# Performance work log

Hardware: AMD Instinct MI355X
Metric: run time of the kernel (lower is better)

The kernel has to match this reference:

```python
import jax, jax.numpy as jnp
import numpy as np

N, E, F, S, R, H = 10000, 160000, 128, 10, 8, 64
SH_OFF = [0, 1, 4, 9]
SH_DIM = [1, 3, 5, 7]
AVG_NUM_NEIGHBORS = 16.0


def setup_inputs() -> dict:
    key = jax.random.key(0)
    ks = jax.random.split(key, 16)
    species = jax.random.randint(ks[0], (N,), 0, S)
    node_attrs = jax.nn.one_hot(species, S, dtype=jnp.float32)
    node_feats = jax.random.normal(ks[1], (N, F), dtype=jnp.float32)
    edge_attrs = jax.random.normal(ks[2], (E, 16), dtype=jnp.float32)
    edge_feats = jax.random.normal(ks[3], (E, R), dtype=jnp.float32)
    edge_index = jax.random.randint(ks[4], (2, E), 0, N)
    # learned parameters
    W_skip_node = jax.random.normal(ks[5], (F, S, F), dtype=jnp.float32)
    W_up = jax.random.normal(ks[6], (F, F), dtype=jnp.float32)
    mlp_w1 = jax.random.normal(ks[7], (R, H), dtype=jnp.float32)
    mlp_w2 = jax.random.normal(ks[8], (H, H), dtype=jnp.float32)
    mlp_w3 = jax.random.normal(ks[9], (H, H), dtype=jnp.float32)
    mlp_w4 = jax.random.normal(ks[10], (H, 4 * F), dtype=jnp.float32)  # conv_tp.weight_numel = 512
    W_lin = jax.random.normal(ks[11], (4, F, F), dtype=jnp.float32)
    W_skip_msg = jax.random.normal(ks[12], (4, F, S, F), dtype=jnp.float32)
    W_out = jax.random.normal(ks[13], (F, F), dtype=jnp.float32)
    return dict(node_attrs=node_attrs, node_feats=node_feats, edge_attrs=edge_attrs,
                edge_feats=edge_feats, edge_index=edge_index, species=species,
                W_skip_node=W_skip_node, W_up=W_up, mlp_w1=mlp_w1, mlp_w2=mlp_w2,
                mlp_w3=mlp_w3, mlp_w4=mlp_w4, W_lin=W_lin, W_skip_msg=W_skip_msg,
                W_out=W_out)


def reference(node_attrs, node_feats, edge_attrs, edge_feats, edge_index, species,
              W_skip_node, W_up, mlp_w1, mlp_w2, mlp_w3, mlp_w4,
              W_lin, W_skip_msg, W_out):
    sender, receiver = edge_index[0], edge_index[1]
    num_nodes = node_feats.shape[0]
    num_edges = edge_attrs.shape[0]

    # skip_tp_node: FullyConnectedTensorProduct(128x0e, 10x0e -> 128x0e), fan_in = 128*10
    skip = jnp.einsum('nu,nv,uvw->nw', node_feats, node_attrs, W_skip_node) * (1.0 / np.sqrt(F * S))

    # linear_up: 128x0e -> 128x0e
    h = (node_feats @ W_up) * (1.0 / np.sqrt(F))

    # radial MLP (e3nn FullyConnectedNet: no bias, w/sqrt(fan_in), silu on hidden layers)
    t = edge_feats
    for W in (mlp_w1, mlp_w2, mlp_w3):
        t = jax.nn.silu((t @ W) * (1.0 / np.sqrt(W.shape[0])))
    tp_w = (t @ mlp_w4) * (1.0 / np.sqrt(H))  # [E, 512]

    # conv_tp (gather -> 0e x l -> l 'uvu' TP) fused with scatter_sum per l-block
    hs = h[sender]  # [E, 128]
    msgs = []
    for l in range(4):
        d = SH_DIM[l]
        w_l = tp_w[:, l * F:(l + 1) * F]                       # [E, 128]
        sh_l = edge_attrs[:, SH_OFF[l]:SH_OFF[l] + d]          # [E, d]
        mji = (hs * w_l)[:, :, None] * sh_l[:, None, :]        # [E, 128, d]
        m = jax.ops.segment_sum(mji.reshape(num_edges, F * d), receiver,
                                num_segments=num_nodes)
        msgs.append(m.reshape(num_nodes, F, d))

    inv_avg = 1.0 / np.sqrt(AVG_NUM_NEIGHBORS)
    # linear (per-l 128->128) / sqrt(avg_num_neighbors), then skip_tp_msg (x 10x0e attrs)
    blocks = []
    for l in range(4):
        x = jnp.einsum('num,uw->nwm', msgs[l], W_lin[l]) * (inv_avg / np.sqrt(F))
        x = jnp.einsum('num,nv,uvw->nwm', x, node_attrs, W_skip_msg[l]) * (1.0 / np.sqrt(F * S))
        blocks.append(x)

    # linear_out: target -> 128x0e keeps only the scalar (l=0) block
    message = (blocks[0][:, :, 0] @ W_out) * (1.0 / np.sqrt(F))  # [N, 128]
    return message, skip
```

## Files before the change

kernel.cpp:

```cpp
#include <hip/hip_runtime.h>
#include <math.h>

#define NFEAT 128
#define NSPEC 10

__global__ void k_hist(const int* __restrict__ species, int* __restrict__ counts, int N) {
    int i = blockIdx.x * blockDim.x + threadIdx.x;
    if (i < N) atomicAdd(&counts[species[i]], 1);
}

__global__ void k_build(const int* __restrict__ counts, int* __restrict__ cursor,
                        int4* __restrict__ table, int* __restrict__ nTiles) {
    if (threadIdx.x == 0 && blockIdx.x == 0) {
        int off = 0, nt = 0;
        for (int s = 0; s < NSPEC; s++) {
            cursor[s] = off;
            int c = counts[s];
            for (int b = 0; b < c; b += 64)
                table[nt++] = make_int4(s, off + b, min(64, c - b), 0);
            off += c;
        }
        nTiles[0] = nt;
    }
}

__global__ void k_scatter(const int* __restrict__ species, int* __restrict__ cursor,
                          int* __restrict__ sorted, int N) {
    int i = blockIdx.x * blockDim.x + threadIdx.x;
    if (i < N) {
        int p = atomicAdd(&cursor[species[i]], 1);
        sorted[p] = i;
    }
}

__global__ void k_ehist(const int* __restrict__ edge_index, int* __restrict__ ehist, int E) {
    int i = blockIdx.x * blockDim.x + threadIdx.x;
    if (i < E) atomicAdd(&ehist[edge_index[E + i]], 1);
}

__global__ void k_escan(const int* __restrict__ ehist, int* __restrict__ estart,
                        int* __restrict__ ecursor, int N) {
    __shared__ int ssum[256];
    const int t = threadIdx.x;
    const int chunk = (N + 255) / 256;
    const int lo = t * chunk;
    const int hi = min(lo + chunk, N);
    int local = 0;
    for (int i = lo; i < hi; i++) local += ehist[i];
    ssum[t] = local;
    __syncthreads();
    for (int off = 1; off < 256; off <<= 1) {
        int x = (t >= off) ? ssum[t - off] : 0;
        __syncthreads();
        ssum[t] += x;
        __syncthreads();
    }
    int run = ssum[t] - local;
    for (int i = lo; i < hi; i++) {
        estart[i] = run;
        ecursor[i] = run;
        run += ehist[i];
    }
}

__global__ void k_escatter(const int* __restrict__ edge_index, int* __restrict__ ecursor,
                           int* __restrict__ eorder, int E) {
    int i = blockIdx.x * blockDim.x + threadIdx.x;
    if (i < E) {
        int r = edge_index[E + i];
        int p = atomicAdd(&ecursor[r], 1);
        eorder[p] = i;
    }
}

__global__ __launch_bounds__(256) void k_gemm(
    const float* __restrict__ A, int aStride,
    const float* __restrict__ B, int bStride, int bSpecStride,
    float* __restrict__ C, int cStride, int cChunkY,
    int M, float alpha,
    const int* __restrict__ sorted,
    const int4* __restrict__ table,
    const int* __restrict__ nTiles)
{
    __shared__ float At[128][64];
    __shared__ float Bs[128][128];
    const int t = threadIdx.x;
    const int gy = blockIdx.y;

    int start, cnt, spec = 0;
    if (table) {
        if (blockIdx.x >= nTiles[0]) return;
        int4 te = table[blockIdx.x];
        spec = te.x; start = te.y; cnt = te.z;
    } else {
        start = blockIdx.x * 64;
        cnt = M - start;
        if (cnt <= 0) return;
        if (cnt > 64) cnt = 64;
    }

    {
        const float* Bp = B + (long)spec * bSpecStride + (long)gy * 128;
        #pragma unroll
        for (int i = 0; i < 16; i++) {
            int idx = t + 256 * i;
            int k = idx >> 5;
            int c = (idx & 31) * 4;
            *(float4*)&Bs[k][c] = *(const float4*)(Bp + (long)k * bStride + c);
        }
    }
    {
        int r = t & 63;
        int kc = (t >> 6) * 32;
        if (r < cnt) {
            int grow = table ? sorted[start + r] : (start + r);
            const float4* src = (const float4*)(A + (long)grow * aStride + kc);
            #pragma unroll
            for (int i = 0; i < 8; i++) {
                float4 v = src[i];
                At[kc + 4*i + 0][r] = v.x;
                At[kc + 4*i + 1][r] = v.y;
                At[kc + 4*i + 2][r] = v.z;
                At[kc + 4*i + 3][r] = v.w;
            }
        } else {
            #pragma unroll
            for (int i = 0; i < 32; i++) At[kc + i][r] = 0.0f;
        }
    }
    __syncthreads();

    const int c0 = (t & 31) * 4;
    const int r0 = (t >> 5) * 8;
    float acc[8][4] = {};
    #pragma unroll 8
    for (int k = 0; k < 128; k++) {
        float4 b  = *(const float4*)&Bs[k][c0];
        float4 a0 = *(const float4*)&At[k][r0];
        float4 a1 = *(const float4*)&At[k][r0 + 4];
        float av[8] = {a0.x, a0.y, a0.z, a0.w, a1.x, a1.y, a1.z, a1.w};
        #pragma unroll
        for (int i = 0; i < 8; i++) {
            acc[i][0] += av[i] * b.x;
            acc[i][1] += av[i] * b.y;
            acc[i][2] += av[i] * b.z;
            acc[i][3] += av[i] * b.w;
        }
    }
    #pragma unroll
    for (int i = 0; i < 8; i++) {
        int r = r0 + i;
        if (r < cnt) {
            int grow = table ? sorted[start + r] : (start + r);
            float4 v = make_float4(acc[i][0] * alpha, acc[i][1] * alpha,
                                   acc[i][2] * alpha, acc[i][3] * alpha);
            *(float4*)&C[(long)gy * cChunkY + (long)grow * cStride + c0] = v;
        }
    }
}

template <int MODE>
__global__ __launch_bounds__(256) void k_edge(
    const float* __restrict__ edge_attrs,
    const float* __restrict__ edge_feats,
    const int*   __restrict__ edge_index,
    const int*   __restrict__ eorder,
    const float* __restrict__ W1,
    const float* __restrict__ W2,
    const float* __restrict__ W3,
    const float* __restrict__ W4,
    const float* __restrict__ h,
    float*       __restrict__ wmsg,
    float*       __restrict__ msgs0,
    int E)
{
    __shared__ float W1s[8][64];
    __shared__ float W2s[64][64];
    __shared__ float W3s[64][64];
    __shared__ float efT[8][64];
    __shared__ float taT[64][64];
    __shared__ float tbT[64][64];
    __shared__ int   sendS[64];
    __shared__ int   recvS[64];
    __shared__ float sh0S[64];

    const int t = threadIdx.x;
    if (t < 128) ((float4*)W1s)[t] = ((const float4*)W1)[t];
    #pragma unroll
    for (int i = 0; i < 4; i++) {
        ((float4*)W2s)[t + 256 * i] = ((const float4*)W2)[t + 256 * i];
        ((float4*)W3s)[t + 256 * i] = ((const float4*)W3)[t + 256 * i];
    }
    __syncthreads();

    const float s1 = 0.3535533905932738f;
    const float s2 = 0.125f;

    const int e0 = (t & 15) * 4;
    const int j0 = (t >> 4) * 4;

    int ntiles = (E + 63) >> 6;
    for (int tile = blockIdx.x; tile < ntiles; tile += gridDim.x) {
        int ebase = tile << 6;
        if (t < 64) {
            int p = ebase + t;
            if (p < E) {
                int e = (MODE == 1) ? eorder[p] : p;
                sendS[t] = edge_index[e];
                recvS[t] = edge_index[E + e];
                sh0S[t]  = edge_attrs[(long)e * 16];
            } else { sendS[t] = 0; recvS[t] = -1; sh0S[t] = 0.0f; }
        } else if (t < 128) {
            int l = t - 64;
            int p = ebase + l;
            if (p < E) {
                int e = (MODE == 1) ? eorder[p] : p;
                const float4* src = (const float4*)(edge_feats + (long)e * 8);
                float4 v0 = src[0], v1 = src[1];
                efT[0][l] = v0.x; efT[1][l] = v0.y; efT[2][l] = v0.z; efT[3][l] = v0.w;
                efT[4][l] = v1.x; efT[5][l] = v1.y; efT[6][l] = v1.z; efT[7][l] = v1.w;
            } else {
                #pragma unroll
                for (int k = 0; k < 8; k++) efT[k][l] = 0.0f;
            }
        }
        __syncthreads();

        {
            float acc[4][4] = {};
            #pragma unroll
            for (int k = 0; k < 8; k++) {
                float4 a = *(const float4*)&efT[k][e0];
                float4 b = *(const float4*)&W1s[k][j0];
                float av[4] = {a.x, a.y, a.z, a.w};
                float bv[4] = {b.x, b.y, b.z, b.w};
                #pragma unroll
                for (int jj = 0; jj < 4; jj++)
                    #pragma unroll
                    for (int ee = 0; ee < 4; ee++)
                        acc[jj][ee] += av[ee] * bv[jj];
            }
            #pragma unroll
            for (int jj = 0; jj < 4; jj++) {
                float4 v; float x;
                x = acc[jj][0] * s1; v.x = x / (1.0f + expf(-x));
                x = acc[jj][1] * s1; v.y = x / (1.0f + expf(-x));
                x = acc[jj][2] * s1; v.z = x / (1.0f + expf(-x));
                x = acc[jj][3] * s1; v.w = x / (1.0f + expf(-x));
                *(float4*)&taT[j0 + jj][e0] = v;
            }
        }
        __syncthreads();

        {
            float acc[4][4] = {};
            #pragma unroll 4
            for (int k = 0; k < 64; k++) {
                float4 a = *(const float4*)&taT[k][e0];
                float4 b = *(const float4*)&W2s[k][j0];
                float av[4] = {a.x, a.y, a.z, a.w};
                float bv[4] = {b.x, b.y, b.z, b.w};
                #pragma unroll
                for (int jj = 0; jj < 4; jj++)
                    #pragma unroll
                    for (int ee = 0; ee < 4; ee++)
                        acc[jj][ee] += av[ee] * bv[jj];
            }
            #pragma unroll
            for (int jj = 0; jj < 4; jj++) {
                float4 v; float x;
                x = acc[jj][0] * s2; v.x = x / (1.0f + expf(-x));
                x = acc[jj][1] * s2; v.y = x / (1.0f + expf(-x));
                x = acc[jj][2] * s2; v.z = x / (1.0f + expf(-x));
                x = acc[jj][3] * s2; v.w = x / (1.0f + expf(-x));
                *(float4*)&tbT[j0 + jj][e0] = v;
            }
        }
        __syncthreads();

        {
            float acc[4][4] = {};
            #pragma unroll 4
            for (int k = 0; k < 64; k++) {
                float4 a = *(const float4*)&tbT[k][e0];
                float4 b = *(const float4*)&W3s[k][j0];
                float av[4] = {a.x, a.y, a.z, a.w};
                float bv[4] = {b.x, b.y, b.z, b.w};
                #pragma unroll
                for (int jj = 0; jj < 4; jj++)
                    #pragma unroll
                    for (int ee = 0; ee < 4; ee++)
                        acc[jj][ee] += av[ee] * bv[jj];
            }
            #pragma unroll
            for (int jj = 0; jj < 4; jj++) {
                float4 v; float x;
                x = acc[jj][0] * s2; v.x = x / (1.0f + expf(-x));
                x = acc[jj][1] * s2; v.y = x / (1.0f + expf(-x));
                x = acc[jj][2] * s2; v.z = x / (1.0f + expf(-x));
                x = acc[jj][3] * s2; v.w = x / (1.0f + expf(-x));
                *(float4*)&taT[j0 + jj][e0] = v;
            }
        }
        __syncthreads();

        {
            const int c0  = (t & 31) * 4;
            const int ew0 = (t >> 5) * 8;
            float acc[8][4] = {};
            #pragma unroll 4
            for (int k = 0; k < 64; k++) {
                float4 b  = *(const float4*)&W4[k * 512 + c0];
                float4 a0 = *(const float4*)&taT[k][ew0];
                float4 a1 = *(const float4*)&taT[k][ew0 + 4];
                float av[8] = {a0.x, a0.y, a0.z, a0.w, a1.x, a1.y, a1.z, a1.w};
                #pragma unroll
                for (int i = 0; i < 8; i++) {
                    acc[i][0] += av[i] * b.x;
                    acc[i][1] += av[i] * b.y;
                    acc[i][2] += av[i] * b.z;
                    acc[i][3] += av[i] * b.w;
                }
            }
            if (MODE == 0) {
                #pragma unroll
                for (int i = 0; i < 8; i++) {
                    int el = ew0 + i;
                    int e  = ebase + el;
                    if (e < E) {
                        float f = sh0S[el] * s2;
                        int snd = sendS[el];
                        float4 hv = *(const float4*)&h[(long)snd * NFEAT + c0];
                        float4 v = make_float4(acc[i][0] * f * hv.x, acc[i][1] * f * hv.y,
                                               acc[i][2] * f * hv.z, acc[i][3] * f * hv.w);
                        *(float4*)&wmsg[(long)e * NFEAT + c0] = v;
                    }
                }
            } else {
                float4 sum = make_float4(0.f, 0.f, 0.f, 0.f);
                int cur = recvS[ew0];
                #pragma unroll
                for (int i = 0; i < 8; i++) {
                    int el = ew0 + i;
                    int rcv = recvS[el];
                    float f = sh0S[el] * s2;
                    int snd = sendS[el];
                    float4 hv = *(const float4*)&h[(long)snd * NFEAT + c0];
                    float4 v = make_float4(acc[i][0] * f * hv.x, acc[i][1] * f * hv.y,
                                           acc[i][2] * f * hv.z, acc[i][3] * f * hv.w);
                    if (rcv != cur) {
                        if (cur >= 0) {
                            float* dst = msgs0 + (long)cur * NFEAT + c0;
                            atomicAdd(dst + 0, sum.x); atomicAdd(dst + 1, sum.y);
                            atomicAdd(dst + 2, sum.z); atomicAdd(dst + 3, sum.w);
                        }
                        cur = rcv; sum = v;
                    } else {
                        sum.x += v.x; sum.y += v.y; sum.z += v.z; sum.w += v.w;
                    }
                }
                if (cur >= 0) {
                    float* dst = msgs0 + (long)cur * NFEAT + c0;
                    atomicAdd(dst + 0, sum.x); atomicAdd(dst + 1, sum.y);
                    atomicAdd(dst + 2, sum.z); atomicAdd(dst + 3, sum.w);
                }
            }
        }
        __syncthreads();
    }
}

__global__ __launch_bounds__(256) void k_gather(
    const float* __restrict__ wmsg, const int* __restrict__ estart,
    const int* __restrict__ ehist, const int* __restrict__ eorder,
    float* __restrict__ msgs0, int N)
{
    int w = (blockIdx.x * blockDim.x + threadIdx.x) >> 6;
    int lane = threadIdx.x & 63;
    int totalWaves = (gridDim.x * blockDim.x) >> 6;
    for (int r = w; r < N; r += totalWaves) {
        int s = estart[r], c = ehist[r];
        float2 sum = make_float2(0.f, 0.f);
        for (int i = 0; i < c; i++) {
            int e = eorder[s + i];
            float2 v = *(const float2*)&wmsg[(long)e * NFEAT + lane * 2];
            sum.x += v.x; sum.y += v.y;
        }
        *(float2*)&msgs0[(long)r * NFEAT + lane * 2] = sum;
    }
}

extern "C" void kernel_launch(void* const* d_in, const int* in_sizes, int n_in,
                              void* d_out, int out_size, void* d_ws, size_t ws_size,
                              hipStream_t stream) {
    const float* node_feats = (const float*)d_in[1];
    const float* edge_attrs = (const float*)d_in[2];
    const float* edge_feats = (const float*)d_in[3];
    const int*   edge_index = (const int*)  d_in[4];
    const int*   species    = (const int*)  d_in[5];
    const float* Wsn        = (const float*)d_in[6];
    const float* Wup        = (const float*)d_in[7];
    const float* W1         = (const float*)d_in[8];
    const float* W2         = (const float*)d_in[9];
    const float* W3         = (const float*)d_in[10];
    const float* W4         = (const float*)d_in[11];
    const float* Wlin       = (const float*)d_in[12];
    const float* Wsm        = (const float*)d_in[13];
    const float* Wout       = (const float*)d_in[14];

    const int N = in_sizes[5];
    const int E = in_sizes[4] / 2;
    const int NF = NFEAT;

    float* out     = (float*)d_out;
    float* message = out;
    float* skip    = out + (long)N * NF;

    char* wsb = (char*)d_ws;
    size_t off = 0;
    auto carve = [&](size_t bytes) { void* p = wsb + off; off = (off + bytes + 255) & ~(size_t)255; return p; };
    float* h      = (float*)carve((size_t)N * NF * 4);
    float* msgs0  = (float*)carve((size_t)N * NF * 4);
    float* Tst    = (float*)carve((size_t)NSPEC * NF * NF * 4);
    float* Comb   = (float*)carve((size_t)NSPEC * NF * NF * 4);
    int*   sorted = (int*)carve((size_t)N * 4);
    int*   counts = (int*)carve(64);
    int*   cursor = (int*)carve(64);
    int*   nTiles = (int*)carve(16);
    int4*  table  = (int4*)carve(256 * 16);
    int*   ehist  = (int*)carve((size_t)N * 4);
    int*   estart = (int*)carve((size_t)N * 4);
    int*   ecursor= (int*)carve((size_t)N * 4);
    int*   eorder = (int*)carve((size_t)E * 4);
    size_t needB  = off;
    float* wmsg   = (float*)carve((size_t)E * NF * 4);
    size_t needA  = off;
    const bool useA = (ws_size >= needA);
    (void)needB;

    const float aH    = 1.0f / sqrtf((float)NF);
    const float aSkip = 1.0f / sqrtf((float)(NF * NSPEC));
    const float cTot  = 0.25f / ((float)NF * sqrtf((float)(NF * NSPEC)));

    hipMemsetAsync(counts, 0, 64, stream);
    hipMemsetAsync(ehist, 0, (size_t)N * 4, stream);
    if (!useA) hipMemsetAsync(msgs0, 0, (size_t)N * NF * 4, stream);

    k_hist   <<<(N + 255) / 256, 256, 0, stream>>>(species, counts, N);
    k_build  <<<1, 64, 0, stream>>>(counts, cursor, table, nTiles);
    k_scatter<<<(N + 255) / 256, 256, 0, stream>>>(species, cursor, sorted, N);

    k_ehist   <<<(E + 255) / 256, 256, 0, stream>>>(edge_index, ehist, E);
    k_escan   <<<1, 256, 0, stream>>>(ehist, estart, ecursor, N);
    k_escatter<<<(E + 255) / 256, 256, 0, stream>>>(edge_index, ecursor, eorder, E);

    const int mTiles   = (N + 63) / 64;
    const int maxTiles = mTiles + NSPEC;

    k_gemm<<<dim3(mTiles, 1), 256, 0, stream>>>(
        node_feats, NF, Wup, NF, 0, h, NF, NF, N, aH, nullptr, nullptr, nullptr);

    k_gemm<<<dim3(2, NSPEC), 256, 0, stream>>>(
        Wlin, NF, Wsm, NF * NSPEC, 0, Tst, NF, NF * NF, NF, 1.0f, nullptr, nullptr, nullptr);

    k_gemm<<<dim3((NSPEC * NF) / 64, 1), 256, 0, stream>>>(
        Tst, NF, Wout, NF, 0, Comb, NF, NF, NSPEC * NF, cTot, nullptr, nullptr, nullptr);

    k_gemm<<<dim3(maxTiles, 1), 256, 0, stream>>>(
        node_feats, NF, Wsn, NF * NSPEC, NF, skip, NF, NF, N, aSkip, sorted, table, nTiles);

    int edgeTiles = (E + 63) / 64;
    int edgeGrid  = edgeTiles < 512 ? edgeTiles : 512;
    if (useA) {
        k_edge<0><<<edgeGrid, 256, 0, stream>>>(
            edge_attrs, edge_feats, edge_index, nullptr, W1, W2, W3, W4, h, wmsg, msgs0, E);
        int gBlocks = (N + 3) / 4;
        k_gather<<<gBlocks, 256, 0, stream>>>(wmsg, estart, ehist, eorder, msgs0, N);
    } else {
        k_edge<1><<<edgeGrid, 256, 0, stream>>>(
            edge_attrs, edge_feats, edge_index, eorder, W1, W2, W3, W4, h, nullptr, msgs0, E);
    }

    k_gemm<<<dim3(maxTiles, 1), 256, 0, stream>>>(
        msgs0, NF, Comb, NF, NF * NF, message, NF, NF, N, 1.0f, sorted, table, nTiles);
}
```

Measured before the change: 421.3 us.

## Drop per-edge message buffer in favor of sorted atomic segment reduction; split GEMM columns

Result: faster. 397.6 us (-5.6%).

```diff
diff --git a/kernel.cpp b/kernel.cpp
--- a/kernel.cpp
+++ b/kernel.cpp
@@ -38,8 +38,7 @@
     if (i < E) atomicAdd(&ehist[edge_index[E + i]], 1);
 }
 
-__global__ void k_escan(const int* __restrict__ ehist, int* __restrict__ estart,
-                        int* __restrict__ ecursor, int N) {
+__global__ void k_escan(const int* __restrict__ ehist, int* __restrict__ ecursor, int N) {
     __shared__ int ssum[256];
     const int t = threadIdx.x;
     const int chunk = (N + 255) / 256;
@@ -57,7 +56,6 @@
     }
     int run = ssum[t] - local;
     for (int i = lo; i < hi; i++) {
-        estart[i] = run;
         ecursor[i] = run;
         run += ehist[i];
     }
@@ -73,6 +71,7 @@
     }
 }
 
+template <int BC>
 __global__ __launch_bounds__(256) void k_gemm(
     const float* __restrict__ A, int aStride,
     const float* __restrict__ B, int bStride, int bSpecStride,
@@ -83,7 +82,7 @@
     const int* __restrict__ nTiles)
 {
     __shared__ float At[128][64];
-    __shared__ float Bs[128][128];
+    __shared__ float Bs[128][BC];
     const int t = threadIdx.x;
     const int gy = blockIdx.y;
 
@@ -100,12 +99,13 @@
     }
 
     {
-        const float* Bp = B + (long)spec * bSpecStride + (long)gy * 128;
+        const float* Bp = B + (long)spec * bSpecStride + (long)gy * BC;
+        constexpr int F4R = BC / 4;
         #pragma unroll
-        for (int i = 0; i < 16; i++) {
+        for (int i = 0; i < (128 * F4R) / 256; i++) {
             int idx = t + 256 * i;
-            int k = idx >> 5;
-            int c = (idx & 31) * 4;
+            int k = idx / F4R;
+            int c = (idx % F4R) * 4;
             *(float4*)&Bs[k][c] = *(const float4*)(Bp + (long)k * bStride + c);
         }
     }
@@ -130,17 +130,22 @@
     }
     __syncthreads();
 
-    const int c0 = (t & 31) * 4;
-    const int r0 = (t >> 5) * 8;
-    float acc[8][4] = {};
+    constexpr int CG   = BC / 4;
+    constexpr int ROWS = BC / 16;
+    const int c0 = (t % CG) * 4;
+    const int r0 = (t / CG) * ROWS;
+    float acc[ROWS][4] = {};
     #pragma unroll 8
     for (int k = 0; k < 128; k++) {
-        float4 b  = *(const float4*)&Bs[k][c0];
-        float4 a0 = *(const float4*)&At[k][r0];
-        float4 a1 = *(const float4*)&At[k][r0 + 4];
-        float av[8] = {a0.x, a0.y, a0.z, a0.w, a1.x, a1.y, a1.z, a1.w};
+        float4 b = *(const float4*)&Bs[k][c0];
+        float av[ROWS];
         #pragma unroll
-        for (int i = 0; i < 8; i++) {
+        for (int i = 0; i < ROWS / 4; i++) {
+            float4 a = *(const float4*)&At[k][r0 + 4 * i];
+            av[4*i + 0] = a.x; av[4*i + 1] = a.y; av[4*i + 2] = a.z; av[4*i + 3] = a.w;
+        }
+        #pragma unroll
+        for (int i = 0; i < ROWS; i++) {
             acc[i][0] += av[i] * b.x;
             acc[i][1] += av[i] * b.y;
             acc[i][2] += av[i] * b.z;
@@ -148,7 +153,7 @@
         }
     }
     #pragma unroll
-    for (int i = 0; i < 8; i++) {
+    for (int i = 0; i < ROWS; i++) {
         int r = r0 + i;
         if (r < cnt) {
             int grow = table ? sorted[start + r] : (start + r);
@@ -159,7 +164,6 @@
     }
 }
 
-template <int MODE>
 __global__ __launch_bounds__(256) void k_edge(
     const float* __restrict__ edge_attrs,
     const float* __restrict__ edge_feats,
@@ -170,7 +174,6 @@
     const float* __restrict__ W3,
     const float* __restrict__ W4,
     const float* __restrict__ h,
-    float*       __restrict__ wmsg,
     float*       __restrict__ msgs0,
     int E)
 {
@@ -205,7 +208,7 @@
         if (t < 64) {
             int p = ebase + t;
             if (p < E) {
-                int e = (MODE == 1) ? eorder[p] : p;
+                int e = eorder[p];
                 sendS[t] = edge_index[e];
                 recvS[t] = edge_index[E + e];
                 sh0S[t]  = edge_attrs[(long)e * 16];
@@ -214,7 +217,7 @@
             int l = t - 64;
             int p = ebase + l;
             if (p < E) {
-                int e = (MODE == 1) ? eorder[p] : p;
+                int e = eorder[p];
                 const float4* src = (const float4*)(edge_feats + (long)e * 8);
                 float4 v0 = src[0], v1 = src[1];
                 efT[0][l] = v0.x; efT[1][l] = v0.y; efT[2][l] = v0.z; efT[3][l] = v0.w;
@@ -322,71 +325,35 @@
                     acc[i][3] += av[i] * b.w;
                 }
             }
-            if (MODE == 0) {
-                #pragma unroll
-                for (int i = 0; i < 8; i++) {
-                    int el = ew0 + i;
-                    int e  = ebase + el;
-                    if (e < E) {
-                        float f = sh0S[el] * s2;
-                        int snd = sendS[el];
-                        float4 hv = *(const float4*)&h[(long)snd * NFEAT + c0];
-                        float4 v = make_float4(acc[i][0] * f * hv.x, acc[i][1] * f * hv.y,
-                                               acc[i][2] * f * hv.z, acc[i][3] * f * hv.w);
-                        *(float4*)&wmsg[(long)e * NFEAT + c0] = v;
+            float4 sum = make_float4(0.f, 0.f, 0.f, 0.f);
+            int cur = recvS[ew0];
+            #pragma unroll
+            for (int i = 0; i < 8; i++) {
+                int el = ew0 + i;
+                int rcv = recvS[el];
+                float f = sh0S[el] * s2;
+                int snd = sendS[el];
+                float4 hv = *(const float4*)&h[(long)snd * NFEAT + c0];
+                float4 v = make_float4(acc[i][0] * f * hv.x, acc[i][1] * f * hv.y,
+                                       acc[i][2] * f * hv.z, acc[i][3] * f * hv.w);
+                if (rcv != cur) {
+                    if (cur >= 0) {
+                        float* dst = msgs0 + (long)cur * NFEAT + c0;
+                        atomicAdd(dst + 0, sum.x); atomicAdd(dst + 1, sum.y);
+                        atomicAdd(dst + 2, sum.z); atomicAdd(dst + 3, sum.w);
                     }
+                    cur = rcv; sum = v;
+                } else {
+                    sum.x += v.x; sum.y += v.y; sum.z += v.z; sum.w += v.w;
                 }
-            } else {
-                float4 sum = make_float4(0.f, 0.f, 0.f, 0.f);
-                int cur = recvS[ew0];
-                #pragma unroll
-                for (int i = 0; i < 8; i++) {
-                    int el = ew0 + i;
-                    int rcv = recvS[el];
-                    float f = sh0S[el] * s2;
-                    int snd = sendS[el];
-                    float4 hv = *(const float4*)&h[(long)snd * NFEAT + c0];
-                    float4 v = make_float4(acc[i][0] * f * hv.x, acc[i][1] * f * hv.y,
-                                           acc[i][2] * f * hv.z, acc[i][3] * f * hv.w);
-                    if (rcv != cur) {
-                        if (cur >= 0) {
-                            float* dst = msgs0 + (long)cur * NFEAT + c0;
-                            atomicAdd(dst + 0, sum.x); atomicAdd(dst + 1, sum.y);
-                            atomicAdd(dst + 2, sum.z); atomicAdd(dst + 3, sum.w);
-                        }
-                        cur = rcv; sum = v;
-                    } else {
-                        sum.x += v.x; sum.y += v.y; sum.z += v.z; sum.w += v.w;
-                    }
-                }
-                if (cur >= 0) {
-                    float* dst = msgs0 + (long)cur * NFEAT + c0;
-                    atomicAdd(dst + 0, sum.x); atomicAdd(dst + 1, sum.y);
-                    atomicAdd(dst + 2, sum.z); atomicAdd(dst + 3, sum.w);
-                }
-            }
-        }
-        __syncthreads();
-    }
-}
-
-__global__ __launch_bounds__(256) void k_gather(
-    const float* __restrict__ wmsg, const int* __restrict__ estart,
-    const int* __restrict__ ehist, const int* __restrict__ eorder,
-    float* __restrict__ msgs0, int N)
-{
-    int w = (blockIdx.x * blockDim.x + threadIdx.x) >> 6;
-    int lane = threadIdx.x & 63;
-    int totalWaves = (gridDim.x * blockDim.x) >> 6;
-    for (int r = w; r < N; r += totalWaves) {
-        int s = estart[r], c = ehist[r];
-        float2 sum = make_float2(0.f, 0.f);
-        for (int i = 0; i < c; i++) {
-            int e = eorder[s + i];
-            float2 v = *(const float2*)&wmsg[(long)e * NFEAT + lane * 2];
-            sum.x += v.x; sum.y += v.y;
-        }
-        *(float2*)&msgs0[(long)r * NFEAT + lane * 2] = sum;
+            }
+            if (cur >= 0) {
+                float* dst = msgs0 + (long)cur * NFEAT + c0;
+                atomicAdd(dst + 0, sum.x); atomicAdd(dst + 1, sum.y);
+                atomicAdd(dst + 2, sum.z); atomicAdd(dst + 3, sum.w);
+            }
+        }
+        __syncthreads();
     }
 }
 
@@ -429,14 +396,8 @@
     int*   nTiles = (int*)carve(16);
     int4*  table  = (int4*)carve(256 * 16);
     int*   ehist  = (int*)carve((size_t)N * 4);
-    int*   estart = (int*)carve((size_t)N * 4);
     int*   ecursor= (int*)carve((size_t)N * 4);
     int*   eorder = (int*)carve((size_t)E * 4);
-    size_t needB  = off;
-    float* wmsg   = (float*)carve((size_t)E * NF * 4);
-    size_t needA  = off;
-    const bool useA = (ws_size >= needA);
-    (void)needB;
 
     const float aH    = 1.0f / sqrtf((float)NF);
     const float aSkip = 1.0f / sqrtf((float)(NF * NSPEC));
@@ -444,43 +405,36 @@
 
     hipMemsetAsync(counts, 0, 64, stream);
     hipMemsetAsync(ehist, 0, (size_t)N * 4, stream);
-    if (!useA) hipMemsetAsync(msgs0, 0, (size_t)N * NF * 4, stream);
+    hipMemsetAsync(msgs0, 0, (size_t)N * NF * 4, stream);
 
     k_hist   <<<(N + 255) / 256, 256, 0, stream>>>(species, counts, N);
     k_build  <<<1, 64, 0, stream>>>(counts, cursor, table, nTiles);
     k_scatter<<<(N + 255) / 256, 256, 0, stream>>>(species, cursor, sorted, N);
 
     k_ehist   <<<(E + 255) / 256, 256, 0, stream>>>(edge_index, ehist, E);
-    k_escan   <<<1, 256, 0, stream>>>(ehist, estart, ecursor, N);
+    k_escan   <<<1, 256, 0, stream>>>(ehist, ecursor, N);
     k_escatter<<<(E + 255) / 256, 256, 0, stream>>>(edge_index, ecursor, eorder, E);
 
     const int mTiles   = (N + 63) / 64;
     const int maxTiles = mTiles + NSPEC;
 
-    k_gemm<<<dim3(mTiles, 1), 256, 0, stream>>>(
-        node_feats, NF, Wup, NF, 0, h, NF, NF, N, aH, nullptr, nullptr, nullptr);
-
-    k_gemm<<<dim3(2, NSPEC), 256, 0, stream>>>(
+    k_gemm<64><<<dim3(mTiles, 2), 256, 0, stream>>>(
+        node_feats, NF, Wup, NF, 0, h, NF, 64, N, aH, nullptr, nullptr, nullptr);
+
+    k_gemm<128><<<dim3(2, NSPEC), 256, 0, stream>>>(
         Wlin, NF, Wsm, NF * NSPEC, 0, Tst, NF, NF * NF, NF, 1.0f, nullptr, nullptr, nullptr);
 
-    k_gemm<<<dim3((NSPEC * NF) / 64, 1), 256, 0, stream>>>(
+    k_gemm<128><<<dim3((NSPEC * NF) / 64, 1), 256, 0, stream>>>(
         Tst, NF, Wout, NF, 0, Comb, NF, NF, NSPEC * NF, cTot, nullptr, nullptr, nullptr);
 
-    k_gemm<<<dim3(maxTiles, 1), 256, 0, stream>>>(
-        node_feats, NF, Wsn, NF * NSPEC, NF, skip, NF, NF, N, aSkip, sorted, table, nTiles);
+    k_gemm<64><<<dim3(maxTiles, 2), 256, 0, stream>>>(
+        node_feats, NF, Wsn, NF * NSPEC, NF, skip, NF, 64, N, aSkip, sorted, table, nTiles);
 
     int edgeTiles = (E + 63) / 64;
     int edgeGrid  = edgeTiles < 512 ? edgeTiles : 512;
-    if (useA) {
-        k_edge<0><<<edgeGrid, 256, 0, stream>>>(
-            edge_attrs, edge_feats, edge_index, nullptr, W1, W2, W3, W4, h, wmsg, msgs0, E);
-        int gBlocks = (N + 3) / 4;
-        k_gather<<<gBlocks, 256, 0, stream>>>(wmsg, estart, ehist, eorder, msgs0, N);
-    } else {
-        k_edge<1><<<edgeGrid, 256, 0, stream>>>(
-            edge_attrs, edge_feats, edge_index, eorder, W1, W2, W3, W4, h, nullptr, msgs0, E);
-    }
-
-    k_gemm<<<dim3(maxTiles, 1), 256, 0, stream>>>(
-        msgs0, NF, Comb, NF, NF * NF, message, NF, NF, N, 1.0f, sorted, table, nTiles);
-}
+    k_edge<<<edgeGrid, 256, 0, stream>>>(
+        edge_attrs, edge_feats, edge_index, eorder, W1, W2, W3, W4, h, msgs0, E);
+
+    k_gemm<64><<<dim3(maxTiles, 2), 256, 0, stream>>>(
+        msgs0, NF, Comb, NF, NF * NF, message, NF, 64, N, 1.0f, sorted, table, nTiles);
+}
```
